# Performance work log

Hardware: AMD Instinct MI355X
Metric: run time of the kernel (lower is better)

## Reference

```python
import jax, jax.numpy as jnp
import numpy as np
from jax import lax

CUT = 20            # voxel grid per side, hard-coded in the torch module
N, P, OP = 32, 8192, 2048


def _w(key, shape, fan_in):
    return jax.random.normal(key, shape, dtype=jnp.float32) * np.float32(1.0 / np.sqrt(fan_in))


def setup_inputs() -> dict:
    key = jax.random.key(0)
    ks = jax.random.split(key, 20)
    inp = {}
    inp["sc"] = jax.random.uniform(ks[0], (N, P, 2), dtype=jnp.float32, minval=-0.5, maxval=0.5)
    inp["oc"] = jax.random.uniform(ks[1], (N, OP, 2), dtype=jnp.float32, minval=-0.5, maxval=0.5)
    inp["pos"] = jax.random.uniform(ks[2], (N, 2), dtype=jnp.float32, minval=-0.5, maxval=0.5)
    # voxel PointNet MLP (1x1 Conv1d == per-point linear)
    inp["mlp_w1"] = _w(ks[3], (128, 2), 2);        inp["mlp_b1"] = jnp.zeros((128,), jnp.float32)
    inp["mlp_w2"] = _w(ks[4], (256, 128), 128);    inp["mlp_b2"] = jnp.zeros((256,), jnp.float32)
    # dense conv pyramid
    inp["conv1_w"] = _w(ks[5], (512, 256, 3, 3), 256 * 9);   inp["conv1_b"] = jnp.zeros((512,), jnp.float32)
    inp["conv2_w"] = _w(ks[6], (1024, 512, 3, 3), 512 * 9);  inp["conv2_b"] = jnp.zeros((1024,), jnp.float32)
    inp["convt_w"] = _w(ks[7], (512, 1024, 2, 2), 1024 * 4); inp["convt_b"] = jnp.zeros((512,), jnp.float32)
    # object set-abstraction (stack of 1x1 Conv1d)
    inp["sa_w1"] = _w(ks[8], (64, 2), 2);          inp["sa_b1"] = jnp.zeros((64,), jnp.float32)
    inp["sa_w2"] = _w(ks[9], (128, 64), 64);       inp["sa_b2"] = jnp.zeros((128,), jnp.float32)
    inp["sa_w3"] = _w(ks[10], (256, 128), 128);    inp["sa_b3"] = jnp.zeros((256,), jnp.float32)
    inp["sa_w4"] = _w(ks[11], (512, 256), 256);    inp["sa_b4"] = jnp.zeros((512,), jnp.float32)
    # per-cell classifier
    inp["cls_w1"] = _w(ks[12], (1024, 1538), 1538); inp["cls_b1"] = jnp.zeros((1024,), jnp.float32)
    inp["cls_w2"] = _w(ks[13], (256, 1024), 1024);  inp["cls_b2"] = jnp.zeros((256,), jnp.float32)
    inp["cls_w3"] = _w(ks[14], (1, 256), 256);      inp["cls_b3"] = jnp.zeros((1,), jnp.float32)
    return inp


def _conv2d(x, w, b):
    y = lax.conv_general_dilated(x, w, (1, 1), ((1, 1), (1, 1)),
                                 dimension_numbers=("NCHW", "OIHW", "NCHW"))
    return y + b[None, :, None, None]


def _maxpool2(x):
    return lax.reduce_window(x, -jnp.inf, lax.max, (1, 1, 2, 2), (1, 1, 2, 2), "VALID")


def reference(sc, oc, pos,
              mlp_w1, mlp_b1, mlp_w2, mlp_b2,
              conv1_w, conv1_b, conv2_w, conv2_b, convt_w, convt_b,
              sa_w1, sa_b1, sa_w2, sa_b2, sa_w3, sa_b3, sa_w4, sa_b4,
              cls_w1, cls_b1, cls_w2, cls_b2, cls_w3, cls_b3):
    n = sc.shape[0]
    # ---- fused voxelization + PointNet + scatter-max (replaces triple loop) ----
    x, y = sc[..., 0], sc[..., 1]
    # torch condition: cut[i] < x <= cut[i+1] on linspace(-0.5, 0.5, 21)
    bi = jnp.clip(jnp.ceil((x + 0.5) * CUT) - 1, 0, CUT - 1).astype(jnp.int32)
    bj = jnp.clip(jnp.ceil((y + 0.5) * CUT) - 1, 0, CUT - 1).astype(jnp.int32)
    valid = (x > -0.5) & (x <= 0.5) & (y > -0.5) & (y <= 0.5)
    ci = -0.5 + (bi.astype(sc.dtype) + 0.5) / CUT   # voxel center x
    cj = -0.5 + (bj.astype(sc.dtype) + 0.5) / CUT   # voxel center y
    pc = jnp.stack([x - ci, y - cj], axis=-1).reshape(-1, 2)        # [n*P, 2]
    h = jax.nn.relu(pc @ mlp_w1.T + mlp_b1)
    feat = jax.nn.relu(h @ mlp_w2.T + mlp_b2)                       # [n*P, 256]
    seg = jnp.where(valid,
                    jnp.arange(n, dtype=jnp.int32)[:, None] * (CUT * CUT) + bi * CUT + bj,
                    n * CUT * CUT).reshape(-1)                      # invalid -> dummy bin
    nseg = n * CUT * CUT + 1
    mx = jax.ops.segment_max(feat, seg, num_segments=nseg)
    cnt = jax.ops.segment_sum(jnp.ones((n * P,), jnp.float32), seg, num_segments=nseg)
    vox = jnp.where(cnt[:, None] > 0, mx, 0.0)[: n * CUT * CUT]     # empty voxels stay 0
    vox = vox.reshape(n, CUT, CUT, 256).transpose(0, 3, 1, 2)       # [n,256,20,20]
    # ---- dense conv pyramid ----
    f1 = _maxpool2(jax.nn.relu(_conv2d(vox, conv1_w, conv1_b)))     # [n,512,10,10]
    f2 = _maxpool2(jax.nn.relu(_conv2d(f1, conv2_w, conv2_b)))      # [n,1024,5,5]
    f3 = lax.conv_transpose(f2, convt_w, (2, 2), "VALID",
                            dimension_numbers=("NCHW", "OIHW", "NCHW"))
    f3 = f3 + convt_b[None, :, None, None]                          # [n,512,10,10]
    scene = jnp.concatenate([f1, f3], axis=1)                       # [n,1024,10,10]
    S = scene.shape[2]
    scene_flat = scene.reshape(n, 1024, S * S)
    # ---- object PointNet (1x1 convs == per-point linears) + global max ----
    obj_c = oc - jnp.mean(oc, axis=1, keepdims=True)                # [n,OP,2]
    g = jax.nn.relu(obj_c @ sa_w1.T + sa_b1)
    g = jax.nn.relu(g @ sa_w2.T + sa_b2)
    g = jax.nn.relu(g @ sa_w3.T + sa_b3)
    g = jax.nn.relu(g @ sa_w4.T + sa_b4)                            # [n,OP,512]
    obj = jnp.max(g, axis=1)                                        # [n,512]
    obj_tiled = jnp.broadcast_to(obj[:, :, None], (n, 512, S * S))
    # ---- relative position grid ----
    c = -0.5 + (jnp.arange(S, dtype=sc.dtype) + 0.5) / S
    rel_x = jnp.broadcast_to(pos[:, 0][:, None, None] - c[None, :, None], (n, S, S))
    rel_y = jnp.broadcast_to(pos[:, 1][:, None, None] - c[None, None, :], (n, S, S))
    rel = jnp.stack([rel_x, rel_y], axis=1).reshape(n, 2, S * S)
    # ---- per-cell classifier ----
    cin = jnp.concatenate([scene_flat, obj_tiled, rel], axis=1).transpose(0, 2, 1)  # [n,100,1538]
    h = jax.nn.relu(cin @ cls_w1.T + cls_b1)
    h = jax.nn.relu(h @ cls_w2.T + cls_b2)
    return h @ cls_w3.T + cls_b3                                    # [n,100,1]
```

## Files before the change

kernel.cpp:

```cpp
#include <hip/hip_runtime.h>

#define NB 32
#define PP 8192
#define OPP 2048

typedef _Float16 f16;
typedef f16 half8 __attribute__((ext_vector_type(8)));
typedef f16 half4 __attribute__((ext_vector_type(4)));
typedef f16 half2v __attribute__((ext_vector_type(2)));
typedef float f32x4 __attribute__((ext_vector_type(4)));

#define MFMA16(a, b, c) __builtin_amdgcn_mfma_f32_16x16x32_f16(a, b, c, 0, 0, 0)

template <int CO, int CI>
__global__ __launch_bounds__(256) void wfragprep_k(const float* __restrict__ wsrc,
                                                   f16* __restrict__ wf) {
  __shared__ float tile[CI * 9];
  int co = blockIdx.x, t = threadIdx.x;
  const float* src = wsrc + (size_t)co * CI * 9;
  for (int i = t; i < CI * 9; i += 256) tile[i] = src[i];
  __syncthreads();
  constexpr int NBB = CO / 16;
  int nb = co >> 4, l16 = co & 15;
  for (int e = t; e < (CI / 32) * 9 * 4; e += 256) {
    int quad = e & 3;
    int kk = (e >> 2) % 9;
    int cic = e / 36;
    half8 v;
#pragma unroll
    for (int j = 0; j < 8; ++j) {
      int ci = cic * 32 + quad * 8 + j;
      v[j] = (f16)tile[ci * 9 + kk];
    }
    *(half8*)(wf + ((((size_t)cic * 9 + kk) * NBB + nb) * 64 + quad * 16 + l16) * 8) = v;
  }
}

__global__ void cvt16_k(const float* __restrict__ in, f16* __restrict__ out, int n4) {
  int idx = blockIdx.x * 256 + threadIdx.x;
  if (idx >= n4) return;
  float4 v = ((const float4*)in)[idx];
  half4 h; h.x = (f16)v.x; h.y = (f16)v.y; h.z = (f16)v.z; h.w = (f16)v.w;
  ((half4*)out)[idx] = h;
}

__global__ void cw1prep_k(const float* __restrict__ w, f16* __restrict__ out) {
  int idx = blockIdx.x * 256 + threadIdx.x;
  if (idx >= 1024 * 1024) return;
  int co = idx >> 10, k = idx & 1023;
  out[idx] = (f16)w[(size_t)co * 1538 + k];
}

__global__ void ctprep_k(const float* __restrict__ w, f16* __restrict__ out) {
  int idx = blockIdx.x * 256 + threadIdx.x;
  if (idx >= 2048 * 1024) return;
  int j = idx & 7, l = (idx >> 3) & 63, kb = (idx >> 9) & 31, nb = idx >> 14;
  int n16 = l & 15, quad = l >> 4;
  int np = nb * 16 + n16;
  int k = kb * 32 + quad * 8 + j;
  int p = np >> 9, o = np & 511;
  out[idx] = (f16)w[((size_t)o * 1024 + k) * 4 + (3 - p)];
}

__global__ void ocmean_k(const float* __restrict__ oc, float* __restrict__ ocm) {
  int n = blockIdx.x, t = threadIdx.x;
  __shared__ float sx[256], sy[256];
  float ax = 0.f, ay = 0.f;
  for (int p = t; p < OPP; p += 256) {
    ax += oc[((size_t)n * OPP + p) * 2 + 0];
    ay += oc[((size_t)n * OPP + p) * 2 + 1];
  }
  sx[t] = ax; sy[t] = ay;
  __syncthreads();
  for (int s = 128; s > 0; s >>= 1) {
    if (t < s) { sx[t] += sx[t + s]; sy[t] += sy[t + s]; }
    __syncthreads();
  }
  if (t == 0) {
    ocm[n * 2 + 0] = sx[0] / (float)OPP;
    ocm[n * 2 + 1] = sy[0] / (float)OPP;
  }
}

__global__ __launch_bounds__(256) void pointnet_lds_k(
    const float* __restrict__ sc, const float* __restrict__ w1, const float* __restrict__ b1,
    const f16* __restrict__ w2h, const float* __restrict__ b2, float* __restrict__ voxg) {
  __shared__ float voxl[400 * 33];
  int t = threadIdx.x, lane = t & 63, w = t >> 6;
  int quad = lane >> 4, l16 = lane & 15;
  int b = blockIdx.x;
  int ps = b & 3, cg = (b >> 2) & 7, n = b >> 5;
  half2v w1x2[16], w1y2[16], b12[16];
#pragma unroll
  for (int i = 0; i < 16; ++i) {
    int k0 = (i >> 2) * 32 + quad * 8 + (i & 3) * 2;
    w1x2[i] = (half2v){(f16)w1[k0 * 2], (f16)w1[(k0 + 1) * 2]};
    w1y2[i] = (half2v){(f16)w1[k0 * 2 + 1], (f16)w1[(k0 + 1) * 2 + 1]};
    b12[i]  = (half2v){(f16)b1[k0], (f16)b1[k0 + 1]};
  }
  half8 bf[2][4];
  float bias[2];
#pragma unroll
  for (int nt = 0; nt < 2; ++nt) {
    int ch = cg * 32 + nt * 16 + l16;
    bias[nt] = b2[ch];
#pragma unroll
    for (int ks = 0; ks < 4; ++ks)
      bf[nt][ks] = *(const half8*)(w2h + (size_t)ch * 128 + ks * 32 + quad * 8);
  }
  for (int i = t; i < 400 * 33; i += 256) voxl[i] = 0.0f;
  __syncthreads();
  const half2v z2 = {};
  const float* scp = sc + ((size_t)n * PP + (size_t)ps * 2048) * 2;
  int p0 = w * 16 + l16;
  float2 xy = *(const float2*)(scp + p0 * 2);
  for (int it = 0; it < 32; ++it) {
    float x = xy.x, y = xy.y;
    if (it < 31) xy = *(const float2*)(scp + ((it + 1) * 64 + p0) * 2);
    float bif = fminf(fmaxf(ceilf((x + 0.5f) * 20.0f) - 1.0f, 0.0f), 19.0f);
    float bjf = fminf(fmaxf(ceilf((y + 0.5f) * 20.0f) - 1.0f, 0.0f), 19.0f);
    bool valid = (x > -0.5f) && (x <= 0.5f) && (y > -0.5f) && (y <= 0.5f);
    float px = x - (-0.5f + (bif + 0.5f) * 0.05f);
    float py = y - (-0.5f + (bjf + 0.5f) * 0.05f);
    int bn = valid ? ((int)bif * 20 + (int)bjf) : -1;
    f16 pxh = (f16)px, pyh = (f16)py;
    half2v px2 = (half2v){pxh, pxh}, py2 = (half2v){pyh, pyh};
    f32x4 acc0 = {}, acc1 = {};
#pragma unroll
    for (int ks = 0; ks < 4; ++ks) {
      half8 af;
#pragma unroll
      for (int j2 = 0; j2 < 4; ++j2) {
        half2v tmp = w1x2[ks * 4 + j2] * px2 + (w1y2[ks * 4 + j2] * py2 + b12[ks * 4 + j2]);
        tmp = __builtin_elementwise_max(tmp, z2);
        reinterpret_cast<half2v*>(&af)[j2] = tmp;
      }
      acc0 = MFMA16(af, bf[0][ks], acc0);
      acc1 = MFMA16(af, bf[1][ks], acc1);
    }
#pragma unroll
    for (int r = 0; r < 4; ++r) {
      int bn2 = __shfl(bn, quad * 4 + r);
      if (bn2 >= 0) {
        float v0 = fmaxf(acc0[r] + bias[0], 0.0f);
        float v1 = fmaxf(acc1[r] + bias[1], 0.0f);
        atomicMax((int*)voxl + bn2 * 33 + l16, __float_as_int(v0));
        atomicMax((int*)voxl + bn2 * 33 + 16 + l16, __float_as_int(v1));
      }
    }
  }
  __syncthreads();
  float* vg = voxg + ((size_t)n * 400) * 256 + cg * 32;
  for (int i = t; i < 400 * 32; i += 256) {
    int bin = i >> 5, c = i & 31;
    float v = voxl[bin * 33 + c];
    if (v > 0.0f)
      atomicMax((int*)(vg + (size_t)bin * 256) + c, __float_as_int(v));
  }
}

template <int H, int W, int CI, int CO, int MSPLIT>
__global__ __launch_bounds__(256, 2) void convmfma_k(
    const f16* __restrict__ inh, const f16* __restrict__ wf,
    const float* __restrict__ bias, f16* __restrict__ outh) {
  constexpr int HS = H / MSPLIT;
  constexpr int Mpix = HS * W;
  constexpr int MT = (Mpix + 15) / 16;
  constexpr int PR = HS + 2, PC = W + 2;
  constexpr int NCIC = CI / 32;
  constexpr int COG = CO / 128;
  constexpr int NBB = CO / 16;
  extern __shared__ char smem[];
  f16* Ap = (f16*)smem;
  int b = blockIdx.x;
  int cog = b % COG;
  int ms = (b / COG) % MSPLIT;
  int n = b / (COG * MSPLIT);
  int co0 = cog * 128;
  int r0 = ms * HS;
  int t = threadIdx.x, lane = t & 63, w = t >> 6;
  int quad = lane >> 4, l16 = lane & 15;
  int nb0 = cog * 8 + w * 2;

  int abase[MT];
#pragma unroll
  for (int mi = 0; mi < MT; ++mi) {
    int pl = mi * 16 + l16; if (pl > Mpix - 1) pl = Mpix - 1;
    int y = pl / W, x = pl - y * W;
    abase[mi] = (y * PC + x) * 40 + quad * 8;
  }
  f32x4 acc[MT][2] = {};

  const f16* inbase = inh + (size_t)n * H * W * CI;

  for (int cic = 0; cic < NCIC; ++cic) {
    __syncthreads();
    for (int cell = t; cell < PR * PC; cell += 256) {
      int pr = cell / PC, pc = cell - pr * PC;
      int yin = r0 - 1 + pr, xin = pc - 1;
      uint4 d0 = {0,0,0,0}, d1 = {0,0,0,0}, d2 = {0,0,0,0}, d3 = {0,0,0,0};
      if (yin >= 0 && yin < H && xin >= 0 && xin < W) {
        const uint4* src = (const uint4*)(inbase + ((size_t)yin * W + xin) * CI + cic * 32);
        d0 = src[0]; d1 = src[1]; d2 = src[2]; d3 = src[3];
      }
      uint4* dst = (uint4*)(Ap + cell * 40);
      dst[0] = d0; dst[1] = d1; dst[2] = d2; dst[3] = d3;
    }
    __syncthreads();
    const f16* wfc = wf + (size_t)(cic * 9) * NBB * 512;
#pragma unroll
    for (int ky = 0; ky < 3; ++ky)
#pragma unroll
      for (int kx = 0; kx < 3; ++kx) {
        int kk = ky * 3 + kx;
        half8 bf0 = *(const half8*)(wfc + ((size_t)(kk * NBB + nb0) * 64 + lane) * 8);
        half8 bf1 = *(const half8*)(wfc + ((size_t)(kk * NBB + nb0 + 1) * 64 + lane) * 8);
        int shift = (ky * PC + kx) * 40;
#pragma unroll
        for (int mi = 0; mi < MT; ++mi) {
          half8 af = *(const half8*)(Ap + abase[mi] + shift);
          acc[mi][0] = MFMA16(af, bf0, acc[mi][0]);
          acc[mi][1] = MFMA16(af, bf1, acc[mi][1]);
        }
      }
  }
  int co_w = co0 + w * 32;
  float bv0 = bias[co_w + l16];
  float bv1 = bias[co_w + 16 + l16];
  f16* ob = outh + ((size_t)n * H * W + (size_t)ms * Mpix) * CO;
#pragma unroll
  for (int mi = 0; mi < MT; ++mi) {
#pragma unroll
    for (int r = 0; r < 4; ++r) {
      int p = mi * 16 + quad * 4 + r;
      if (p < Mpix) {
        float v0 = acc[mi][0][r] + bv0; v0 = v0 > 0.f ? v0 : 0.f;
        float v1 = acc[mi][1][r] + bv1; v1 = v1 > 0.f ? v1 : 0.f;
        ob[(size_t)p * CO + co_w + l16] = (f16)v0;
        ob[(size_t)p * CO + co_w + 16 + l16] = (f16)v1;
      }
    }
  }
}

__global__ void pool1_k(const f16* __restrict__ g1, f16* __restrict__ f1h,
                        f16* __restrict__ scnh) {
  int idx = blockIdx.x * 256 + threadIdx.x;
  if (idx >= 32 * 100 * 256) return;
  int c2 = idx & 255, rem = idx >> 8;
  int op = rem % 100, n = rem / 100;
  int py = op / 10, px = op - py * 10;
  const f16* base = g1 + (((size_t)n * 400 + (size_t)(2 * py) * 20 + 2 * px) * 512) + c2 * 2;
  float a0 = (float)base[0],   a1 = (float)base[1];
  float b0 = (float)base[512], b1 = (float)base[513];
  const f16* base2 = base + 20 * 512;
  float c0 = (float)base2[0],   c1 = (float)base2[1];
  float d0 = (float)base2[512], d1 = (float)base2[513];
  union { f16 h[2]; unsigned u; } pk;
  pk.h[0] = (f16)fmaxf(fmaxf(a0, b0), fmaxf(c0, d0));
  pk.h[1] = (f16)fmaxf(fmaxf(a1, b1), fmaxf(c1, d1));
  *(unsigned*)(f1h + ((size_t)n * 100 + op) * 512 + c2 * 2) = pk.u;
  *(unsigned*)(scnh + ((size_t)n * 100 + op) * 1024 + c2 * 2) = pk.u;
}

__global__ void pool2_k(const f16* __restrict__ g2, f16* __restrict__ f2h) {
  int idx = blockIdx.x * 256 + threadIdx.x;
  if (idx >= 32 * 25 * 512) return;
  int c2 = idx & 511, rem = idx >> 9;
  int op = rem % 25, n = rem / 25;
  int py = op / 5, px = op - py * 5;
  const f16* base = g2 + (((size_t)n * 100 + (size_t)(2 * py) * 10 + 2 * px) * 1024) + c2 * 2;
  float a0 = (float)base[0],    a1 = (float)base[1];
  float b0 = (float)base[1024], b1 = (float)base[1025];
  const f16* base2 = base + 10 * 1024;
  float c0 = (float)base2[0],    c1 = (float)base2[1];
  float d0 = (float)base2[1024], d1 = (float)base2[1025];
  f16* o = f2h + ((size_t)n * 25 + op) * 1024 + c2 * 2;
  o[0] = (f16)fmaxf(fmaxf(a0, b0), fmaxf(c0, d0));
  o[1] = (f16)fmaxf(fmaxf(a1, b1), fmaxf(c1, d1));
}

__global__ __launch_bounds__(256, 2) void convt_mfma_k(
    const f16* __restrict__ f2h, const f16* __restrict__ ctwf,
    const float* __restrict__ ctb, f16* __restrict__ scnh) {
  __shared__ f16 act[25 * 1048];
  int b = blockIdx.x;
  int ng = b & 15, n = b >> 4;
  int t = threadIdx.x, lane = t & 63, w = t >> 6;
  int quad = lane >> 4, l16 = lane & 15;
  for (int i = t; i < 25 * 128; i += 256) {
    int row = i >> 7, c8 = i & 127;
    *(half8*)(act + row * 1048 + c8 * 8) =
        *(const half8*)(f2h + ((size_t)n * 25 + row) * 1024 + c8 * 8);
  }
  __syncthreads();
  int r1 = 16 + (l16 > 8 ? 8 : l16);
  f32x4 acc[2][2] = {};
  const f16* wp0 = ctwf + ((size_t)((ng * 8 + w * 2 + 0) * 32) * 64 + lane) * 8;
  const f16* wp1 = ctwf + ((size_t)((ng * 8 + w * 2 + 1) * 32) * 64 + lane) * 8;
#pragma unroll 4
  for (int ks = 0; ks < 32; ++ks) {
    half8 a0 = *(const half8*)(act + l16 * 1048 + ks * 32 + quad * 8);
    half8 a1 = *(const half8*)(act + r1 * 1048 + ks * 32 + quad * 8);
    half8 b0 = *(const half8*)(wp0 + (size_t)ks * 512);
    half8 b1 = *(const half8*)(wp1 + (size_t)ks * 512);
    acc[0][0] = MFMA16(a0, b0, acc[0][0]);
    acc[1][0] = MFMA16(a1, b0, acc[1][0]);
    acc[0][1] = MFMA16(a0, b1, acc[0][1]);
    acc[1][1] = MFMA16(a1, b1, acc[1][1]);
  }
#pragma unroll
  for (int nt = 0; nt < 2; ++nt) {
    int np = ng * 128 + w * 32 + nt * 16 + l16;
    int p = np >> 9, co = np & 511;
    int a = p >> 1, bc = p & 1;
    float bb = ctb[co];
#pragma unroll
    for (int mt = 0; mt < 2; ++mt)
#pragma unroll
      for (int r = 0; r < 4; ++r) {
        int px = mt * 16 + quad * 4 + r;
        if (px < 25) {
          int ph = px / 5, pw = px - ph * 5;
          int opx = (2 * ph + a) * 10 + 2 * pw + bc;
          scnh[((size_t)n * 100 + opx) * 1024 + 512 + co] = (f16)(acc[mt][nt][r] + bb);
        }
      }
  }
}

__global__ __launch_bounds__(256, 2) void sa_mfma_k(
    const float* __restrict__ oc, const float* __restrict__ ocm,
    const float* __restrict__ w1, const float* __restrict__ b1,
    const f16* __restrict__ w2h, const float* __restrict__ b2,
    const f16* __restrict__ w3h, const float* __restrict__ b3,
    const f16* __restrict__ w4h, const float* __restrict__ b4,
    float* __restrict__ obj) {
  __shared__ f16 act1[64 * 72];
  __shared__ f16 act2[64 * 136];
  __shared__ f16 act3[64 * 264];
  __shared__ float pcx[64], pcy[64];
  int b = blockIdx.x;
  int n = b >> 5, pb = (b & 31) * 64;
  int t = threadIdx.x, lane = t & 63, w = t >> 6;
  int quad = lane >> 4, l16 = lane & 15;
  if (t < 64) {
    pcx[t] = oc[((size_t)n * OPP + pb + t) * 2 + 0] - ocm[n * 2 + 0];
    pcy[t] = oc[((size_t)n * OPP + pb + t) * 2 + 1] - ocm[n * 2 + 1];
  }
  __syncthreads();
  {
    int c = t & 63, pg = t >> 6;
    float wx = w1[c * 2], wy = w1[c * 2 + 1], bb = b1[c];
#pragma unroll
    for (int j = 0; j < 16; ++j) {
      int p = pg * 16 + j;
      act1[p * 72 + c] = (f16)fmaxf(fmaf(wx, pcx[p], fmaf(wy, pcy[p], bb)), 0.0f);
    }
  }
  __syncthreads();
  {
    int n0 = w * 32;
    f32x4 acc[4][2] = {};
#pragma unroll
    for (int ks = 0; ks < 2; ++ks) {
      half8 a[4];
#pragma unroll
      for (int mt = 0; mt < 4; ++mt)
        a[mt] = *(const half8*)(act1 + (mt * 16 + l16) * 72 + ks * 32 + quad * 8);
#pragma unroll
      for (int nt = 0; nt < 2; ++nt) {
        half8 bf = *(const half8*)(w2h + (size_t)(n0 + nt * 16 + l16) * 64 + ks * 32 + quad * 8);
#pragma unroll
        for (int mt = 0; mt < 4; ++mt)
          acc[mt][nt] = MFMA16(a[mt], bf, acc[mt][nt]);
      }
    }
#pragma unroll
    for (int nt = 0; nt < 2; ++nt) {
      int col = n0 + nt * 16 + l16;
      float bb = b2[col];
#pragma unroll
      for (int mt = 0; mt < 4; ++mt)
#pragma unroll
        for (int r = 0; r < 4; ++r)
          act2[(mt * 16 + quad * 4 + r) * 136 + col] = (f16)fmaxf(acc[mt][nt][r] + bb, 0.0f);
    }
  }
  __syncthreads();
  {
    int n0 = w * 64;
    f32x4 acc[4][4] = {};
#pragma unroll
    for (int ks = 0; ks < 4; ++ks) {
      half8 a[4];
#pragma unroll
      for (int mt = 0; mt < 4; ++mt)
        a[mt] = *(const half8*)(act2 + (mt * 16 + l16) * 136 + ks * 32 + quad * 8);
#pragma unroll
      for (int nt = 0; nt < 4; ++nt) {
        half8 bf = *(const half8*)(w3h + (size_t)(n0 + nt * 16 + l16) * 128 + ks * 32 + quad * 8);
#pragma unroll
        for (int mt = 0; mt < 4; ++mt)
          acc[mt][nt] = MFMA16(a[mt], bf, acc[mt][nt]);
      }
    }
#pragma unroll
    for (int nt = 0; nt < 4; ++nt) {
      int col = n0 + nt * 16 + l16;
      float bb = b3[col];
#pragma unroll
      for (int mt = 0; mt < 4; ++mt)
#pragma unroll
        for (int r = 0; r < 4; ++r)
          act3[(mt * 16 + quad * 4 + r) * 264 + col] = (f16)fmaxf(acc[mt][nt][r] + bb, 0.0f);
    }
  }
  __syncthreads();
  {
    int n0 = w * 128;
    f32x4 acc[4][8] = {};
#pragma unroll
    for (int ks = 0; ks < 8; ++ks) {
      half8 a[4];
#pragma unroll
      for (int mt = 0; mt < 4; ++mt)
        a[mt] = *(const half8*)(act3 + (mt * 16 + l16) * 264 + ks * 32 + quad * 8);
#pragma unroll
      for (int nt = 0; nt < 8; ++nt) {
        half8 bf = *(const half8*)(w4h + (size_t)(n0 + nt * 16 + l16) * 256 + ks * 32 + quad * 8);
#pragma unroll
        for (int mt = 0; mt < 4; ++mt)
          acc[mt][nt] = MFMA16(a[mt], bf, acc[mt][nt]);
      }
    }
#pragma unroll
    for (int nt = 0; nt < 8; ++nt) {
      int col = n0 + nt * 16 + l16;
      float bb = b4[col];
      float v = 0.0f;
#pragma unroll
      for (int mt = 0; mt < 4; ++mt)
#pragma unroll
        for (int r = 0; r < 4; ++r)
          v = fmaxf(v, acc[mt][nt][r] + bb);
      v = fmaxf(v, 0.0f);
      v = fmaxf(v, __shfl_xor(v, 16));
      v = fmaxf(v, __shfl_xor(v, 32));
      if (quad == 0)
        atomicMax((int*)obj + (size_t)n * 512 + col, __float_as_int(v));
    }
  }
}

__global__ __launch_bounds__(256) void odprep_k(
    const float* __restrict__ obj, const float* __restrict__ w1raw,
    const float* __restrict__ b1, float* __restrict__ odw, float* __restrict__ wab) {
  int co = blockIdx.x;
  int t = threadIdx.x, lane = t & 63, w = t >> 6;
  const float* wr = w1raw + (size_t)co * 1538 + 1024;
  float2 wv[4];
#pragma unroll
  for (int j = 0; j < 4; ++j) wv[j] = *(const float2*)(wr + lane * 8 + j * 2);
  float bb = b1[co];
  for (int i = 0; i < 8; ++i) {
    int n = w * 8 + i;
    const float* ob = obj + (size_t)n * 512 + lane * 8;
    float od = 0.0f;
#pragma unroll
    for (int j = 0; j < 4; ++j) {
      float2 ov = *(const float2*)(ob + j * 2);
      od = fmaf(wv[j].x, ov.x, od);
      od = fmaf(wv[j].y, ov.y, od);
    }
    od += __shfl_xor(od, 1);  od += __shfl_xor(od, 2);
    od += __shfl_xor(od, 4);  od += __shfl_xor(od, 8);
    od += __shfl_xor(od, 16); od += __shfl_xor(od, 32);
    if (lane == 0) odw[(size_t)n * 1024 + co] = od + bb;
  }
  if (t == 0) { wab[co * 2] = wr[512]; wab[co * 2 + 1] = wr[513]; }
}

__global__ __launch_bounds__(256) void cls1_mfma_k(
    const f16* __restrict__ scnh, const float* __restrict__ odw,
    const float* __restrict__ wab, const float* __restrict__ pos,
    const f16* __restrict__ w1h, f16* __restrict__ h1h) {
  __shared__ f16 act[25 * 1032];
  __shared__ float odl[128], wAl[128], wBl[128];
  int b = blockIdx.x;
  int o8 = b & 7, mq = (b >> 3) & 3, n = b >> 5;
  int co0 = o8 * 128, p0 = mq * 25;
  int t = threadIdx.x, lane = t & 63, w = t >> 6;
  int quad = lane >> 4, l16 = lane & 15;
  for (int i = t; i < 25 * 128; i += 256) {
    int row = i >> 7, c8 = i & 127;
    *(half8*)(act + row * 1032 + c8 * 8) =
        *(const half8*)(scnh + ((size_t)n * 100 + p0 + row) * 1024 + c8 * 8);
  }
  if (t < 128) {
    odl[t] = odw[(size_t)n * 1024 + co0 + t];
    float2 ab = *(const float2*)(wab + (size_t)(co0 + t) * 2);
    wAl[t] = ab.x; wBl[t] = ab.y;
  }
  __syncthreads();
  float posx = pos[n * 2 + 0], posy = pos[n * 2 + 1];
  f32x4 acc[2][2];
#pragma unroll
  for (int mt = 0; mt < 2; ++mt)
#pragma unroll
    for (int nt = 0; nt < 2; ++nt) {
      int cl = w * 32 + nt * 16 + l16;
      float od = odl[cl], wA = wAl[cl], wB = wBl[cl];
#pragma unroll
      for (int r = 0; r < 4; ++r) {
        int pl = mt * 16 + quad * 4 + r;
        int px = p0 + (pl < 25 ? pl : 24);
        float relx = posx - (-0.5f + ((px / 10) + 0.5f) * 0.1f);
        float rely = posy - (-0.5f + ((px % 10) + 0.5f) * 0.1f);
        acc[mt][nt][r] = od + relx * wA + rely * wB;
      }
    }
  int gr0 = l16;
  int gr1 = (16 + l16 > 24) ? 24 : 16 + l16;
  const f16* wb0 = w1h + (size_t)(co0 + w * 32 + l16) * 1024 + quad * 8;
  const f16* wb1 = wb0 + (size_t)16 * 1024;
#pragma unroll 4
  for (int kq = 0; kq < 32; ++kq) {
    int k0 = kq * 32;
    half8 bf0 = *(const half8*)(wb0 + k0);
    half8 bf1 = *(const half8*)(wb1 + k0);
    half8 a0 = *(const half8*)(act + gr0 * 1032 + k0 + quad * 8);
    half8 a1 = *(const half8*)(act + gr1 * 1032 + k0 + quad * 8);
    acc[0][0] = MFMA16(a0, bf0, acc[0][0]);
    acc[1][0] = MFMA16(a1, bf0, acc[1][0]);
    acc[0][1] = MFMA16(a0, bf1, acc[0][1]);
    acc[1][1] = MFMA16(a1, bf1, acc[1][1]);
  }
#pragma unroll
  for (int mt = 0; mt < 2; ++mt)
#pragma unroll
    for (int nt = 0; nt < 2; ++nt) {
      int co = co0 + w * 32 + nt * 16 + l16;
#pragma unroll
      for (int r = 0; r < 4; ++r) {
        int pl = mt * 16 + quad * 4 + r;
        if (pl < 25)
          h1h[((size_t)n * 100 + p0 + pl) * 1024 + co] = (f16)fmaxf(acc[mt][nt][r], 0.0f);
      }
    }
}

__global__ __launch_bounds__(256) void cls2_mfma_k(
    const f16* __restrict__ h1h, const f16* __restrict__ w2h16,
    const float* __restrict__ b2, f16* __restrict__ h2h) {
  __shared__ f16 act[64 * 72];
  int b = blockIdx.x;
  int ng = b & 1, mh = (b >> 1) & 1, n = b >> 2;
  int co0 = ng * 128, p0 = mh * 50;
  int t = threadIdx.x, lane = t & 63, w = t >> 6;
  int quad = lane >> 4, l16 = lane & 15;
  f32x4 acc[4][2] = {};
  for (int kc = 0; kc < 16; ++kc) {
    int k0 = kc * 64;
    __syncthreads();
    for (int i = t; i < 512; i += 256) {
      int row = i >> 3, c8 = i & 7;
      int gr = p0 + (row < 50 ? row : 49);
      *(half8*)(act + row * 72 + c8 * 8) =
          *(const half8*)(h1h + ((size_t)n * 100 + gr) * 1024 + k0 + c8 * 8);
    }
    __syncthreads();
#pragma unroll
    for (int ks = 0; ks < 2; ++ks) {
      half8 bf0 = *(const half8*)(w2h16 + (size_t)(co0 + w * 32 + l16) * 1024 + k0 + ks * 32 + quad * 8);
      half8 bf1 = *(const half8*)(w2h16 + (size_t)(co0 + w * 32 + 16 + l16) * 1024 + k0 + ks * 32 + quad * 8);
#pragma unroll
      for (int mt = 0; mt < 4; ++mt) {
        half8 a = *(const half8*)(act + (mt * 16 + l16) * 72 + ks * 32 + quad * 8);
        acc[mt][0] = MFMA16(a, bf0, acc[mt][0]);
        acc[mt][1] = MFMA16(a, bf1, acc[mt][1]);
      }
    }
  }
#pragma unroll
  for (int mt = 0; mt < 4; ++mt)
#pragma unroll
    for (int nt = 0; nt < 2; ++nt) {
      int co = co0 + w * 32 + nt * 16 + l16;
      float bb = b2[co];
#pragma unroll
      for (int r = 0; r < 4; ++r) {
        int pl = mt * 16 + quad * 4 + r;
        if (pl < 50)
          h2h[((size_t)n * 100 + p0 + pl) * 256 + co] = (f16)fmaxf(acc[mt][nt][r] + bb, 0.0f);
      }
    }
}

__global__ void cls3_k(const f16* __restrict__ h2h, const float* __restrict__ w3,
                       const float* __restrict__ b3, float* __restrict__ out) {
  int n = blockIdx.x, t = threadIdx.x;
  if (t < 100) {
    float acc = b3[0];
    const f16* hp = &h2h[((size_t)n * 100 + t) * 256];
    for (int k = 0; k < 256; ++k) acc = fmaf((float)hp[k], w3[k], acc);
    out[n * 100 + t] = acc;
  }
}

extern "C" void kernel_launch(void* const* d_in, const int* in_sizes, int n_in,
                              void* d_out, int out_size, void* d_ws, size_t ws_size,
                              hipStream_t stream) {
  const float* sc      = (const float*)d_in[0];
  const float* oc      = (const float*)d_in[1];
  const float* pos     = (const float*)d_in[2];
  const float* mlp_w1  = (const float*)d_in[3];
  const float* mlp_b1  = (const float*)d_in[4];
  const float* mlp_w2  = (const float*)d_in[5];
  const float* mlp_b2  = (const float*)d_in[6];
  const float* conv1_w = (const float*)d_in[7];
  const float* conv1_b = (const float*)d_in[8];
  const float* conv2_w = (const float*)d_in[9];
  const float* conv2_b = (const float*)d_in[10];
  const float* convt_w = (const float*)d_in[11];
  const float* convt_b = (const float*)d_in[12];
  const float* sa_w1   = (const float*)d_in[13];
  const float* sa_b1   = (const float*)d_in[14];
  const float* sa_w2   = (const float*)d_in[15];
  const float* sa_b2   = (const float*)d_in[16];
  const float* sa_w3   = (const float*)d_in[17];
  const float* sa_b3   = (const float*)d_in[18];
  const float* sa_w4   = (const float*)d_in[19];
  const float* sa_b4   = (const float*)d_in[20];
  const float* cls_w1  = (const float*)d_in[21];
  const float* cls_b1  = (const float*)d_in[22];
  const float* cls_w2  = (const float*)d_in[23];
  const float* cls_b2  = (const float*)d_in[24];
  const float* cls_w3  = (const float*)d_in[25];
  const float* cls_b3  = (const float*)d_in[26];

  float* ws = (float*)d_ws;
  f16*   w1h   = (f16*)ws;
  f16*   w2h   = (f16*)(ws + 589824);
  f16*   mw2h  = (f16*)(ws + 2949120);
  f16*   saw2h = (f16*)(ws + 2965504);
  f16*   saw3h = (f16*)(ws + 2969600);
  f16*   saw4h = (f16*)(ws + 2985984);
  f16*   cw1h  = (f16*)(ws + 3051520);
  f16*   ctwh  = (f16*)(ws + 3575808);
  f16*   cw2h  = (f16*)(ws + 4624384);
  float* big   = ws + 4886528;
  f16*   voxh  = (f16*)(ws + 8163328);
  f16*   f1h   = (f16*)(ws + 8982528);
  f16*   scnh  = (f16*)(ws + 9801728);
  float* obj   = ws + 11440128;
  float* ocm   = ws + 11456512;

  float* voxg  = big;
  f16*   g1buf = (f16*)big;
  f16*   g2buf = (f16*)big;
  f16*   f2h   = voxh;
  f16*   h1h   = w2h;
  f16*   h2h   = scnh;
  float* odw   = big + 2097152;
  float* wab   = big + 2129920;
  float* outp  = (float*)d_out;

  wfragprep_k<512, 256><<<512, 256, 0, stream>>>(conv1_w, w1h);
  wfragprep_k<1024, 512><<<1024, 256, 0, stream>>>(conv2_w, w2h);
  cvt16_k<<<32, 256, 0, stream>>>(mlp_w2, mw2h, 8192);
  cvt16_k<<<8, 256, 0, stream>>>(sa_w2, saw2h, 2048);
  cvt16_k<<<32, 256, 0, stream>>>(sa_w3, saw3h, 8192);
  cvt16_k<<<128, 256, 0, stream>>>(sa_w4, saw4h, 32768);
  cw1prep_k<<<4096, 256, 0, stream>>>(cls_w1, cw1h);
  ctprep_k<<<8192, 256, 0, stream>>>(convt_w, ctwh);
  cvt16_k<<<256, 256, 0, stream>>>(cls_w2, cw2h, 65536);

  hipMemsetAsync(obj, 0, (size_t)16384 * 4, stream);
  hipMemsetAsync(voxg, 0, (size_t)3276800 * 4, stream);
  ocmean_k<<<32, 256, 0, stream>>>(oc, ocm);

  pointnet_lds_k<<<1024, 256, 0, stream>>>(sc, mlp_w1, mlp_b1, mw2h, mlp_b2, voxg);
  cvt16_k<<<3200, 256, 0, stream>>>(voxg, voxh, 819200);

  convmfma_k<20, 20, 256, 512, 4><<<512, 256, 7 * 22 * 80, stream>>>(
      voxh, w1h, conv1_b, g1buf);
  pool1_k<<<3200, 256, 0, stream>>>(g1buf, f1h, scnh);
  convmfma_k<10, 10, 512, 1024, 2><<<512, 256, 7 * 12 * 80, stream>>>(
      f1h, w2h, conv2_b, g2buf);
  pool2_k<<<1600, 256, 0, stream>>>(g2buf, f2h);
  convt_mfma_k<<<512, 256, 0, stream>>>(f2h, ctwh, convt_b, scnh);

  sa_mfma_k<<<1024, 256, 0, stream>>>(oc, ocm, sa_w1, sa_b1, saw2h, sa_b2,
                                      saw3h, sa_b3, saw4h, sa_b4, obj);
  odprep_k<<<1024, 256, 0, stream>>>(obj, cls_w1, cls_b1, odw, wab);

  cls1_mfma_k<<<1024, 256, 0, stream>>>(scnh, odw, wab, pos, cw1h, h1h);
  cls2_mfma_k<<<128, 256, 0, stream>>>(h1h, cw2h, cls_b2, h2h);
  cls3_k<<<32, 128, 0, stream>>>(h2h, cls_w3, cls_b3, outp);
}
```

Baseline: 497.7 us.

## Fuse weight-prep kernels and ocmean into one launch, widen pointnet blocks

Merges nine weight conversion/reorder kernels plus the object-coordinate mean into a single block-dispatched kernel. It also relocates obj next to voxg so one memset clears both, and doubles pointnet block size to 512 threads with half as many blocks. The aim is to cut launch overhead and duplicated global atomicMax merging. The trade-off is fewer pointnet blocks, which lowers parallelism, and branchy blocks in the fused prep kernel.

```diff
diff --git a/kernel.cpp b/kernel.cpp
--- a/kernel.cpp
+++ b/kernel.cpp
@@ -12,27 +12,85 @@
 
 #define MFMA16(a, b, c) __builtin_amdgcn_mfma_f32_16x16x32_f16(a, b, c, 0, 0, 0)
 
-template <int CO, int CI>
-__global__ __launch_bounds__(256) void wfragprep_k(const float* __restrict__ wsrc,
-                                                   f16* __restrict__ wf) {
-  __shared__ float tile[CI * 9];
-  int co = blockIdx.x, t = threadIdx.x;
-  const float* src = wsrc + (size_t)co * CI * 9;
-  for (int i = t; i < CI * 9; i += 256) tile[i] = src[i];
-  __syncthreads();
-  constexpr int NBB = CO / 16;
-  int nb = co >> 4, l16 = co & 15;
-  for (int e = t; e < (CI / 32) * 9 * 4; e += 256) {
-    int quad = e & 3;
-    int kk = (e >> 2) % 9;
-    int cic = e / 36;
-    half8 v;
-#pragma unroll
-    for (int j = 0; j < 8; ++j) {
-      int ci = cic * 32 + quad * 8 + j;
-      v[j] = (f16)tile[ci * 9 + kk];
-    }
-    *(half8*)(wf + ((((size_t)cic * 9 + kk) * NBB + nb) * 64 + quad * 16 + l16) * 8) = v;
+__global__ __launch_bounds__(256) void prepfuse_k(
+    const float* __restrict__ mlp_w2, const float* __restrict__ sa_w2,
+    const float* __restrict__ sa_w3, const float* __restrict__ sa_w4,
+    const float* __restrict__ cls_w2, const float* __restrict__ cls_w1,
+    const float* __restrict__ convt_w, const float* __restrict__ conv1_w,
+    const float* __restrict__ conv2_w, const float* __restrict__ oc,
+    f16* __restrict__ mw2h, f16* __restrict__ saw2h, f16* __restrict__ saw3h,
+    f16* __restrict__ saw4h, f16* __restrict__ cw2h, f16* __restrict__ cw1h,
+    f16* __restrict__ ctwh, f16* __restrict__ w1h, f16* __restrict__ w2h,
+    float* __restrict__ ocm) {
+  __shared__ float tile[512 * 9];
+  int bb = blockIdx.x, t = threadIdx.x;
+  if (bb < 2048) {
+    constexpr int B0 = 8192, B1 = B0 + 2048, B2 = B1 + 8192, B3 = B2 + 32768, B4 = B3 + 65536;
+    constexpr int C1e = B4 + 524288;
+    constexpr int TOT = C1e + 2097152;
+    for (int idx = bb * 256 + t; idx < TOT; idx += 2048 * 256) {
+      if (idx < B4) {
+        const float* in; f16* out; int off;
+        if (idx < B0)      { in = mlp_w2; out = mw2h;  off = idx; }
+        else if (idx < B1) { in = sa_w2;  out = saw2h; off = idx - B0; }
+        else if (idx < B2) { in = sa_w3;  out = saw3h; off = idx - B1; }
+        else if (idx < B3) { in = sa_w4;  out = saw4h; off = idx - B2; }
+        else               { in = cls_w2; out = cw2h;  off = idx - B3; }
+        float4 v = ((const float4*)in)[off];
+        half4 h; h.x = (f16)v.x; h.y = (f16)v.y; h.z = (f16)v.z; h.w = (f16)v.w;
+        ((half4*)out)[off] = h;
+      } else if (idx < C1e) {
+        int i = idx - B4;
+        int co = i >> 9, k2 = i & 511;
+        float2 v = *(const float2*)(cls_w1 + (size_t)co * 1538 + k2 * 2);
+        half2v h = {(f16)v.x, (f16)v.y};
+        *(half2v*)(cw1h + (size_t)co * 1024 + k2 * 2) = h;
+      } else {
+        int i = idx - C1e;
+        int j = i & 7, l = (i >> 3) & 63, kb = (i >> 9) & 31, nb = i >> 14;
+        int n16 = l & 15, quad = l >> 4;
+        int np = nb * 16 + n16;
+        int k = kb * 32 + quad * 8 + j;
+        int p = np >> 9, o = np & 511;
+        ctwh[i] = (f16)convt_w[((size_t)o * 1024 + k) * 4 + (3 - p)];
+      }
+    }
+  } else if (bb < 2080) {
+    float* sx = tile; float* sy = tile + 256;
+    int n = bb - 2048;
+    float ax = 0.f, ay = 0.f;
+    for (int p = t; p < OPP; p += 256) {
+      ax += oc[((size_t)n * OPP + p) * 2 + 0];
+      ay += oc[((size_t)n * OPP + p) * 2 + 1];
+    }
+    sx[t] = ax; sy[t] = ay;
+    __syncthreads();
+    for (int s = 128; s > 0; s >>= 1) {
+      if (t < s) { sx[t] += sx[t + s]; sy[t] += sy[t + s]; }
+      __syncthreads();
+    }
+    if (t == 0) {
+      ocm[n * 2 + 0] = sx[0] / (float)OPP;
+      ocm[n * 2 + 1] = sy[0] / (float)OPP;
+    }
+  } else {
+    int co, CI, NBB; const float* src0; f16* wf;
+    if (bb < 2592) { co = bb - 2080; CI = 256; NBB = 32; src0 = conv1_w; wf = w1h; }
+    else           { co = bb - 2592; CI = 512; NBB = 64; src0 = conv2_w; wf = w2h; }
+    const float* src = src0 + (size_t)co * CI * 9;
+    for (int i = t; i < CI * 9; i += 256) tile[i] = src[i];
+    __syncthreads();
+    int nb = co >> 4, l16c = co & 15;
+    int tot = (CI / 32) * 9 * 4;
+    for (int e = t; e < tot; e += 256) {
+      int quad = e & 3;
+      int kk = (e >> 2) % 9;
+      int cic = e / 36;
+      half8 v;
+#pragma unroll
+      for (int j = 0; j < 8; ++j) v[j] = (f16)tile[(cic * 32 + quad * 8 + j) * 9 + kk];
+      *(half8*)(wf + ((((size_t)cic * 9 + kk) * NBB + nb) * 64 + quad * 16 + l16c) * 8) = v;
+    }
   }
 }
 
@@ -44,52 +102,14 @@
   ((half4*)out)[idx] = h;
 }
 
-__global__ void cw1prep_k(const float* __restrict__ w, f16* __restrict__ out) {
-  int idx = blockIdx.x * 256 + threadIdx.x;
-  if (idx >= 1024 * 1024) return;
-  int co = idx >> 10, k = idx & 1023;
-  out[idx] = (f16)w[(size_t)co * 1538 + k];
-}
-
-__global__ void ctprep_k(const float* __restrict__ w, f16* __restrict__ out) {
-  int idx = blockIdx.x * 256 + threadIdx.x;
-  if (idx >= 2048 * 1024) return;
-  int j = idx & 7, l = (idx >> 3) & 63, kb = (idx >> 9) & 31, nb = idx >> 14;
-  int n16 = l & 15, quad = l >> 4;
-  int np = nb * 16 + n16;
-  int k = kb * 32 + quad * 8 + j;
-  int p = np >> 9, o = np & 511;
-  out[idx] = (f16)w[((size_t)o * 1024 + k) * 4 + (3 - p)];
-}
-
-__global__ void ocmean_k(const float* __restrict__ oc, float* __restrict__ ocm) {
-  int n = blockIdx.x, t = threadIdx.x;
-  __shared__ float sx[256], sy[256];
-  float ax = 0.f, ay = 0.f;
-  for (int p = t; p < OPP; p += 256) {
-    ax += oc[((size_t)n * OPP + p) * 2 + 0];
-    ay += oc[((size_t)n * OPP + p) * 2 + 1];
-  }
-  sx[t] = ax; sy[t] = ay;
-  __syncthreads();
-  for (int s = 128; s > 0; s >>= 1) {
-    if (t < s) { sx[t] += sx[t + s]; sy[t] += sy[t + s]; }
-    __syncthreads();
-  }
-  if (t == 0) {
-    ocm[n * 2 + 0] = sx[0] / (float)OPP;
-    ocm[n * 2 + 1] = sy[0] / (float)OPP;
-  }
-}
-
-__global__ __launch_bounds__(256) void pointnet_lds_k(
+__global__ __launch_bounds__(512) void pointnet_lds_k(
     const float* __restrict__ sc, const float* __restrict__ w1, const float* __restrict__ b1,
     const f16* __restrict__ w2h, const float* __restrict__ b2, float* __restrict__ voxg) {
   __shared__ float voxl[400 * 33];
   int t = threadIdx.x, lane = t & 63, w = t >> 6;
   int quad = lane >> 4, l16 = lane & 15;
   int b = blockIdx.x;
-  int ps = b & 3, cg = (b >> 2) & 7, n = b >> 5;
+  int ps = b & 1, cg = (b >> 1) & 7, n = b >> 4;
   half2v w1x2[16], w1y2[16], b12[16];
 #pragma unroll
   for (int i = 0; i < 16; ++i) {
@@ -108,15 +128,15 @@
     for (int ks = 0; ks < 4; ++ks)
       bf[nt][ks] = *(const half8*)(w2h + (size_t)ch * 128 + ks * 32 + quad * 8);
   }
-  for (int i = t; i < 400 * 33; i += 256) voxl[i] = 0.0f;
+  for (int i = t; i < 400 * 33; i += 512) voxl[i] = 0.0f;
   __syncthreads();
   const half2v z2 = {};
-  const float* scp = sc + ((size_t)n * PP + (size_t)ps * 2048) * 2;
+  const float* scp = sc + ((size_t)n * PP + (size_t)ps * 4096) * 2;
   int p0 = w * 16 + l16;
   float2 xy = *(const float2*)(scp + p0 * 2);
   for (int it = 0; it < 32; ++it) {
     float x = xy.x, y = xy.y;
-    if (it < 31) xy = *(const float2*)(scp + ((it + 1) * 64 + p0) * 2);
+    if (it < 31) xy = *(const float2*)(scp + ((it + 1) * 128 + p0) * 2);
     float bif = fminf(fmaxf(ceilf((x + 0.5f) * 20.0f) - 1.0f, 0.0f), 19.0f);
     float bjf = fminf(fmaxf(ceilf((y + 0.5f) * 20.0f) - 1.0f, 0.0f), 19.0f);
     bool valid = (x > -0.5f) && (x <= 0.5f) && (y > -0.5f) && (y <= 0.5f);
@@ -151,7 +171,7 @@
   }
   __syncthreads();
   float* vg = voxg + ((size_t)n * 400) * 256 + cg * 32;
-  for (int i = t; i < 400 * 32; i += 256) {
+  for (int i = t; i < 400 * 32; i += 512) {
     int bin = i >> 5, c = i & 31;
     float v = voxl[bin * 33 + c];
     if (v > 0.0f)
@@ -649,11 +669,11 @@
   f16*   cw1h  = (f16*)(ws + 3051520);
   f16*   ctwh  = (f16*)(ws + 3575808);
   f16*   cw2h  = (f16*)(ws + 4624384);
+  float* obj   = ws + 4870144;
   float* big   = ws + 4886528;
   f16*   voxh  = (f16*)(ws + 8163328);
   f16*   f1h   = (f16*)(ws + 8982528);
   f16*   scnh  = (f16*)(ws + 9801728);
-  float* obj   = ws + 11440128;
   float* ocm   = ws + 11456512;
 
   float* voxg  = big;
@@ -666,21 +686,13 @@
   float* wab   = big + 2129920;
   float* outp  = (float*)d_out;
 
-  wfragprep_k<512, 256><<<512, 256, 0, stream>>>(conv1_w, w1h);
-  wfragprep_k<1024, 512><<<1024, 256, 0, stream>>>(conv2_w, w2h);
-  cvt16_k<<<32, 256, 0, stream>>>(mlp_w2, mw2h, 8192);
-  cvt16_k<<<8, 256, 0, stream>>>(sa_w2, saw2h, 2048);
-  cvt16_k<<<32, 256, 0, stream>>>(sa_w3, saw3h, 8192);
-  cvt16_k<<<128, 256, 0, stream>>>(sa_w4, saw4h, 32768);
-  cw1prep_k<<<4096, 256, 0, stream>>>(cls_w1, cw1h);
-  ctprep_k<<<8192, 256, 0, stream>>>(convt_w, ctwh);
-  cvt16_k<<<256, 256, 0, stream>>>(cls_w2, cw2h, 65536);
-
-  hipMemsetAsync(obj, 0, (size_t)16384 * 4, stream);
-  hipMemsetAsync(voxg, 0, (size_t)3276800 * 4, stream);
-  ocmean_k<<<32, 256, 0, stream>>>(oc, ocm);
-
-  pointnet_lds_k<<<1024, 256, 0, stream>>>(sc, mlp_w1, mlp_b1, mw2h, mlp_b2, voxg);
+  hipMemsetAsync(obj, 0, (size_t)(16384 + 3276800) * 4, stream);
+  prepfuse_k<<<3616, 256, 0, stream>>>(mlp_w2, sa_w2, sa_w3, sa_w4, cls_w2, cls_w1,
+                                       convt_w, conv1_w, conv2_w, oc,
+                                       mw2h, saw2h, saw3h, saw4h, cw2h, cw1h,
+                                       ctwh, w1h, w2h, ocm);
+
+  pointnet_lds_k<<<512, 512, 0, stream>>>(sc, mlp_w1, mlp_b1, mw2h, mlp_b2, voxg);
   cvt16_k<<<3200, 256, 0, stream>>>(voxg, voxh, 819200);
 
   convmfma_k<20, 20, 256, 512, 4><<<512, 256, 7 * 22 * 80, stream>>>(
```

Result: faster. 475.5 us (-4.5%).
